# Optimization experiments

Measured on AMD Instinct MI355X. Metric: run time of the kernel, lower is better.

The kernel has to match this reference:

```python
import jax, jax.numpy as jnp
import numpy as np


def setup_inputs() -> dict:
    key = jax.random.key(0)
    ks = jax.random.split(key, 6)
    B, H, N, BS, W, T, D = 1, 32, 256, 32, 128, 4096, 128
    q = jax.random.normal(ks[0], (B, H, N * BS, D), dtype=jnp.float32)
    k_ctx = jax.random.normal(ks[1], (B, H, T, D), dtype=jnp.float32)
    v_ctx = jax.random.normal(ks[2], (B, H, T, D), dtype=jnp.float32)
    k_draft = jax.random.normal(ks[3], (B, H, N * BS, D), dtype=jnp.float32)
    v_draft = jax.random.normal(ks[4], (B, H, N * BS, D), dtype=jnp.float32)
    anchor_positions = jnp.sort(
        jax.random.randint(ks[5], (B, N), 0, T - BS), axis=-1
    )
    block_keep_mask = jnp.ones((B, N), dtype=bool)
    return {
        "q": q, "k_ctx": k_ctx, "v_ctx": v_ctx,
        "k_draft": k_draft, "v_draft": v_draft,
        "anchor_positions": anchor_positions,
        "block_keep_mask": block_keep_mask,
        "context_window": 128,
    }


def reference(q, k_ctx, v_ctx, k_draft, v_draft,
              anchor_positions, block_keep_mask, context_window):
    # FlashMTP block-sparse attention (FlexAttention mask_mod semantics):
    #   query block i attends to context tokens t in [max(0, a_i - W), a_i - 1]
    #   plus its own draft block (bidirectional); invalid blocks see nothing.
    B, H, Q, D = q.shape
    N = anchor_positions.shape[1]
    bs = Q // N
    T = k_ctx.shape[2]
    W = context_window
    scale = 1.0 / np.sqrt(D).astype(np.float32)

    # sliding context window indices per block: (B, N, W)
    idx = anchor_positions[:, :, None] - W + jnp.arange(W)[None, None, :]
    valid_ctx = idx >= 0  # idx < anchor always holds by construction
    idxc = jnp.clip(idx, 0, T - 1)
    gidx = idxc.reshape(B, 1, N * W, 1)
    k_win = jnp.take_along_axis(k_ctx, gidx, axis=2).reshape(B, H, N, W, D)
    v_win = jnp.take_along_axis(v_ctx, gidx, axis=2).reshape(B, H, N, W, D)

    qb = q.reshape(B, H, N, bs, D)
    kb = k_draft.reshape(B, H, N, bs, D)
    vb = v_draft.reshape(B, H, N, bs, D)

    s_ctx = jnp.einsum('bhnqd,bhnwd->bhnqw', qb, k_win) * scale
    s_blk = jnp.einsum('bhnqd,bhnkd->bhnqk', qb, kb) * scale

    keep = block_keep_mask[:, None, :, None, None]           # (B,1,N,1,1)
    m_ctx = valid_ctx[:, None, :, None, :] & keep            # (B,1,N,1,W)
    m_blk = jnp.broadcast_to(keep, (B, 1, N, 1, bs))         # (B,1,N,1,bs)
    mask = jnp.concatenate([m_ctx, m_blk], axis=-1)
    s = jnp.concatenate([s_ctx, s_blk], axis=-1)
    neg = jnp.asarray(-1e30, s.dtype)
    p = jax.nn.softmax(jnp.where(mask, s, neg), axis=-1)

    v_all = jnp.concatenate([v_win, vb], axis=3)             # (B,H,N,W+bs,D)
    out = jnp.einsum('bhnqk,bhnkd->bhnqd', p, v_all)
    out = out * keep.astype(out.dtype)  # invalid blocks -> zero output
    return out.reshape(B, H, Q, D)
```

## Files before the change

kernel.cpp:

```cpp
#include <hip/hip_runtime.h>

constexpr int H_  = 32;
constexpr int N_  = 256;
constexpr int BS_ = 32;
constexpr int W_  = 128;
constexpr int T_  = 4096;
constexpr int D_  = 128;
constexpr int NQ_ = 8192;
constexpr float SCALE_  = 0.08838834764831845f;
constexpr float L2E_    = 1.4426950408889634f;
constexpr float MFLOOR_ = -1.0e28f;
constexpr float DEFER_  = 8.0f;

typedef __attribute__((ext_vector_type(4))) float f4;
typedef __attribute__((ext_vector_type(4))) short s4;
typedef __attribute__((ext_vector_type(8))) short s8;
typedef __attribute__((ext_vector_type(4))) float fx4;

__device__ __forceinline__ short bfrne(float f) {
  unsigned u = __float_as_uint(f);
  u += 0x7fffu + ((u >> 16) & 1u);
  return (short)(u >> 16);
}

__device__ __forceinline__ void lds_barrier() {
  asm volatile("s_waitcnt lgkmcnt(0)" ::: "memory");
  __builtin_amdgcn_s_barrier();
}

__global__ __launch_bounds__(128, 2)
void mtp_attn_kernel(const float* __restrict__ q,
                     const float* __restrict__ k_ctx,
                     const float* __restrict__ v_ctx,
                     const float* __restrict__ k_draft,
                     const float* __restrict__ v_draft,
                     const int* __restrict__ anchor,
                     const int* __restrict__ keepm,
                     float* __restrict__ out)
{
  int u = blockIdx.x;
  u = (u & 7) * 1024 + (u >> 3);
  const int h = u >> 8;
  const int n = u & 255;

  const int tu   = threadIdx.x;
  const int lane = tu & 63;
  const int wu   = tu >> 6;
  const int l15  = lane & 15;
  const int g    = lane >> 4;
  const int rb   = tu >> 5;
  const int c4   = tu & 31;

  const int A  = anchor[n];
  const int kp = keepm[n];
  const int wm = W_ - A;

  __shared__ __align__(16) unsigned char smem_[17664];
  short* kb = (short*)smem_;
  short* vT = (short*)(smem_ + 8448);

  const float* qrow = q + ((size_t)h * NQ_ + (size_t)n * BS_ + wu * 16 + l15) * D_;
  s8 qb[4];
#pragma unroll
  for (int ks = 0; ks < 4; ++ks) {
    f4 f0 = *reinterpret_cast<const f4*>(qrow + ks * 32 + g * 4);
    f4 f1 = *reinterpret_cast<const f4*>(qrow + ks * 32 + 16 + g * 4);
#pragma unroll
    for (int j = 0; j < 4; ++j) { qb[ks][j] = bfrne(f0[j]); qb[ks][j + 4] = bfrne(f1[j]); }
  }

  const float* kcb = k_ctx + (size_t)h * T_ * D_;
  const float* vcb = v_ctx + (size_t)h * T_ * D_;
  const float* kdb = k_draft + ((size_t)h * NQ_ + (size_t)n * BS_) * D_;
  const float* vdb = v_draft + ((size_t)h * NQ_ + (size_t)n * BS_) * D_;

  f4 kr[8], vr[8];

  auto loadK = [&](int c) {
#pragma unroll
    for (int i = 0; i < 8; ++i) {
      int row = i * 4 + rb;
      const float* src;
      if (c < 4) { int idx = A - W_ + c * 32 + row; idx = idx < 0 ? 0 : idx; src = kcb + (size_t)idx * D_; }
      else       { src = kdb + (size_t)row * D_; }
      kr[i] = reinterpret_cast<const f4*>(src)[c4];
    }
  };
  auto loadV = [&](int c) {
#pragma unroll
    for (int p = 0; p < 2; ++p)
#pragma unroll
      for (int i = 0; i < 4; ++i) {
        int row = p * 16 + rb * 4 + i;
        const float* src;
        if (c < 4) { int idx = A - W_ + c * 32 + row; idx = idx < 0 ? 0 : idx; src = vcb + (size_t)idx * D_; }
        else       { src = vdb + (size_t)row * D_; }
        vr[p * 4 + i] = reinterpret_cast<const f4*>(src)[c4];
      }
  };

  loadK(0); loadV(0);

  float m  = -3.0e38f;
  float ls = 0.0f;
  fx4 oacc[8];
#pragma unroll
  for (int t = 0; t < 8; ++t) oacc[t] = {0.f, 0.f, 0.f, 0.f};

#pragma unroll
  for (int c = 0; c < 5; ++c) {
    lds_barrier();
#pragma unroll
    for (int i = 0; i < 8; ++i) {
      s4 w = { bfrne(kr[i][0]), bfrne(kr[i][1]), bfrne(kr[i][2]), bfrne(kr[i][3]) };
      *reinterpret_cast<s4*>(kb + (i * 4 + rb) * 132 + c4 * 4) = w;
    }
#pragma unroll
    for (int p = 0; p < 2; ++p) {
      int keyl = p * 16 + rb * 4;
#pragma unroll
      for (int j = 0; j < 4; ++j) {
        s4 w = { bfrne(vr[p * 4 + 0][j]), bfrne(vr[p * 4 + 1][j]),
                 bfrne(vr[p * 4 + 2][j]), bfrne(vr[p * 4 + 3][j]) };
        *reinterpret_cast<s4*>(vT + (c4 * 4 + j) * 36 + keyl) = w;
      }
    }
    if (c < 4) { loadK(c + 1); loadV(c + 1); }
    lds_barrier();

    fx4 st[2] = { {0.f,0.f,0.f,0.f}, {0.f,0.f,0.f,0.f} };
    __builtin_amdgcn_s_setprio(1);
#pragma unroll
    for (int ks = 0; ks < 4; ++ks) {
#pragma unroll
      for (int t2 = 0; t2 < 2; ++t2) {
        const short* kpr = kb + (t2 * 16 + l15) * 132 + ks * 32 + g * 4;
        s4 b0 = *reinterpret_cast<const s4*>(kpr);
        s4 b1 = *reinterpret_cast<const s4*>(kpr + 16);
        s8 kf = { b0[0], b0[1], b0[2], b0[3], b1[0], b1[1], b1[2], b1[3] };
        st[t2] = __builtin_amdgcn_mfma_f32_16x16x32_bf16(kf, qb[ks], st[t2], 0, 0, 0);
      }
    }
    __builtin_amdgcn_s_setprio(0);

    float sv[2][4];
    float cm = -3.0e38f;
#pragma unroll
    for (int t2 = 0; t2 < 2; ++t2) {
      int kb0 = c * 32 + t2 * 16 + g * 4;
#pragma unroll
      for (int r = 0; r < 4; ++r) {
        float v = st[t2][r] * SCALE_;
        bool valid = (c == 4) || (kb0 + r >= wm);
        v = valid ? v : -1.0e30f;
        sv[t2][r] = v;
        cm = fmaxf(cm, v);
      }
    }
    cm = fmaxf(cm, __shfl_xor(cm, 16));
    cm = fmaxf(cm, __shfl_xor(cm, 32));

    if (c == 0) {
      m = fmaxf(cm, MFLOOR_);
    } else {
      float pm = fmaxf(m, cm);
      if (!__all(pm - m <= DEFER_)) {
        float mn = fmaxf(pm, MFLOOR_);
        float al = exp2f((m - mn) * L2E_);
        ls *= al;
        float alr[4];
#pragma unroll
        for (int r = 0; r < 4; ++r) alr[r] = __shfl(al, g * 4 + r);
#pragma unroll
        for (int nt = 0; nt < 8; ++nt)
#pragma unroll
          for (int r = 0; r < 4; ++r) oacc[nt][r] *= alr[r];
        m = mn;
      }
    }

    s8 pa;
#pragma unroll
    for (int t2 = 0; t2 < 2; ++t2)
#pragma unroll
      for (int r = 0; r < 4; ++r) {
        float p = exp2f((sv[t2][r] - m) * L2E_);
        ls += p;
        pa[t2 * 4 + r] = bfrne(p);
      }

    __builtin_amdgcn_s_setprio(1);
#pragma unroll
    for (int nt = 0; nt < 8; ++nt) {
      const short* vp = vT + (nt * 16 + l15) * 36 + g * 4;
      s4 b0 = *reinterpret_cast<const s4*>(vp);
      s4 b1 = *reinterpret_cast<const s4*>(vp + 16);
      s8 vb2 = { b0[0], b0[1], b0[2], b0[3], b1[0], b1[1], b1[2], b1[3] };
      oacc[nt] = __builtin_amdgcn_mfma_f32_16x16x32_bf16(pa, vb2, oacc[nt], 0, 0, 0);
    }
    __builtin_amdgcn_s_setprio(0);
  }

  ls += __shfl_xor(ls, 16);
  ls += __shfl_xor(ls, 32);
  float linv[4];
#pragma unroll
  for (int r = 0; r < 4; ++r) {
    float lq = __shfl(ls, g * 4 + r);
    linv[r] = kp ? (1.0f / lq) : 0.0f;
  }
  float* ob = out + ((size_t)h * NQ_ + (size_t)n * BS_ + wu * 16 + g * 4) * D_ + l15;
#pragma unroll
  for (int nt = 0; nt < 8; ++nt)
#pragma unroll
    for (int r = 0; r < 4; ++r)
      ob[(size_t)r * D_ + nt * 16] = oacc[nt][r] * linv[r];
}

extern "C" void kernel_launch(void* const* d_in, const int* in_sizes, int n_in,
                              void* d_out, int out_size, void* d_ws, size_t ws_size,
                              hipStream_t stream) {
  (void)in_sizes; (void)n_in; (void)d_ws; (void)ws_size; (void)out_size;
  const float* q       = (const float*)d_in[0];
  const float* k_ctx   = (const float*)d_in[1];
  const float* v_ctx   = (const float*)d_in[2];
  const float* k_draft = (const float*)d_in[3];
  const float* v_draft = (const float*)d_in[4];
  const int*   anchor  = (const int*)d_in[5];
  const int*   keep    = (const int*)d_in[6];
  float*       out     = (float*)d_out;
  mtp_attn_kernel<<<dim3(8192), dim3(128), 0, stream>>>(
      q, k_ctx, v_ctx, k_draft, v_draft, anchor, keep, out);
}
```

Baseline: 159.5 us.

## Double-buffer K/V register prefetch two chunks ahead and use packed bf16 conversion

```diff
diff --git a/kernel.cpp b/kernel.cpp
--- a/kernel.cpp
+++ b/kernel.cpp
@@ -16,12 +16,15 @@
 typedef __attribute__((ext_vector_type(4))) short s4;
 typedef __attribute__((ext_vector_type(8))) short s8;
 typedef __attribute__((ext_vector_type(4))) float fx4;
-
-__device__ __forceinline__ short bfrne(float f) {
-  unsigned u = __float_as_uint(f);
-  u += 0x7fffu + ((u >> 16) & 1u);
-  return (short)(u >> 16);
-}
+typedef __attribute__((ext_vector_type(2))) int i2;
+
+__device__ __forceinline__ int pack2(float a, float b) {
+  int r;
+  asm("v_cvt_pk_bf16_f32 %0, %1, %2" : "=v"(r) : "v"(a), "v"(b));
+  return r;
+}
+
+union frag_u { int w[4]; s8 v; };
 
 __device__ __forceinline__ void lds_barrier() {
   asm volatile("s_waitcnt lgkmcnt(0)" ::: "memory");
@@ -65,8 +68,10 @@
   for (int ks = 0; ks < 4; ++ks) {
     f4 f0 = *reinterpret_cast<const f4*>(qrow + ks * 32 + g * 4);
     f4 f1 = *reinterpret_cast<const f4*>(qrow + ks * 32 + 16 + g * 4);
-#pragma unroll
-    for (int j = 0; j < 4; ++j) { qb[ks][j] = bfrne(f0[j]); qb[ks][j + 4] = bfrne(f1[j]); }
+    frag_u uq;
+    uq.w[0] = pack2(f0[0], f0[1]); uq.w[1] = pack2(f0[2], f0[3]);
+    uq.w[2] = pack2(f1[0], f1[1]); uq.w[3] = pack2(f1[2], f1[3]);
+    qb[ks] = uq.v;
   }
 
   const float* kcb = k_ctx + (size_t)h * T_ * D_;
@@ -74,19 +79,17 @@
   const float* kdb = k_draft + ((size_t)h * NQ_ + (size_t)n * BS_) * D_;
   const float* vdb = v_draft + ((size_t)h * NQ_ + (size_t)n * BS_) * D_;
 
-  f4 kr[8], vr[8];
-
-  auto loadK = [&](int c) {
+  auto loadK = [&](f4 (&dst)[8], int c) {
 #pragma unroll
     for (int i = 0; i < 8; ++i) {
       int row = i * 4 + rb;
       const float* src;
       if (c < 4) { int idx = A - W_ + c * 32 + row; idx = idx < 0 ? 0 : idx; src = kcb + (size_t)idx * D_; }
       else       { src = kdb + (size_t)row * D_; }
-      kr[i] = reinterpret_cast<const f4*>(src)[c4];
+      dst[i] = reinterpret_cast<const f4*>(src)[c4];
     }
   };
-  auto loadV = [&](int c) {
+  auto loadV = [&](f4 (&dst)[8], int c) {
 #pragma unroll
     for (int p = 0; p < 2; ++p)
 #pragma unroll
@@ -95,11 +98,13 @@
         const float* src;
         if (c < 4) { int idx = A - W_ + c * 32 + row; idx = idx < 0 ? 0 : idx; src = vcb + (size_t)idx * D_; }
         else       { src = vdb + (size_t)row * D_; }
-        vr[p * 4 + i] = reinterpret_cast<const f4*>(src)[c4];
+        dst[p * 4 + i] = reinterpret_cast<const f4*>(src)[c4];
       }
   };
 
-  loadK(0); loadV(0);
+  f4 krA[8], vrA[8], krB[8], vrB[8];
+  loadK(krA, 0); loadV(vrA, 0);
+  loadK(krB, 1); loadV(vrB, 1);
 
   float m  = -3.0e38f;
   float ls = 0.0f;
@@ -109,23 +114,26 @@
 
 #pragma unroll
   for (int c = 0; c < 5; ++c) {
+    f4 (&kr)[8] = (c & 1) ? krB : krA;
+    f4 (&vr)[8] = (c & 1) ? vrB : vrA;
+
     lds_barrier();
 #pragma unroll
     for (int i = 0; i < 8; ++i) {
-      s4 w = { bfrne(kr[i][0]), bfrne(kr[i][1]), bfrne(kr[i][2]), bfrne(kr[i][3]) };
-      *reinterpret_cast<s4*>(kb + (i * 4 + rb) * 132 + c4 * 4) = w;
+      i2 w = { pack2(kr[i][0], kr[i][1]), pack2(kr[i][2], kr[i][3]) };
+      *reinterpret_cast<i2*>(kb + (i * 4 + rb) * 132 + c4 * 4) = w;
     }
 #pragma unroll
     for (int p = 0; p < 2; ++p) {
       int keyl = p * 16 + rb * 4;
 #pragma unroll
       for (int j = 0; j < 4; ++j) {
-        s4 w = { bfrne(vr[p * 4 + 0][j]), bfrne(vr[p * 4 + 1][j]),
-                 bfrne(vr[p * 4 + 2][j]), bfrne(vr[p * 4 + 3][j]) };
-        *reinterpret_cast<s4*>(vT + (c4 * 4 + j) * 36 + keyl) = w;
-      }
-    }
-    if (c < 4) { loadK(c + 1); loadV(c + 1); }
+        i2 w = { pack2(vr[p * 4 + 0][j], vr[p * 4 + 1][j]),
+                 pack2(vr[p * 4 + 2][j], vr[p * 4 + 3][j]) };
+        *reinterpret_cast<i2*>(vT + (c4 * 4 + j) * 36 + keyl) = w;
+      }
+    }
+    if (c < 3) { loadK(kr, c + 2); loadV(vr, c + 2); }
     lds_barrier();
 
     fx4 st[2] = { {0.f,0.f,0.f,0.f}, {0.f,0.f,0.f,0.f} };
@@ -179,15 +187,19 @@
       }
     }
 
-    s8 pa;
+    float pv[8];
 #pragma unroll
     for (int t2 = 0; t2 < 2; ++t2)
 #pragma unroll
       for (int r = 0; r < 4; ++r) {
         float p = exp2f((sv[t2][r] - m) * L2E_);
         ls += p;
-        pa[t2 * 4 + r] = bfrne(p);
-      }
+        pv[t2 * 4 + r] = p;
+      }
+    frag_u up;
+    up.w[0] = pack2(pv[0], pv[1]); up.w[1] = pack2(pv[2], pv[3]);
+    up.w[2] = pack2(pv[4], pv[5]); up.w[3] = pack2(pv[6], pv[7]);
+    s8 pa = up.v;
 
     __builtin_amdgcn_s_setprio(1);
 #pragma unroll
```

New measurement: 158.2 us. Within noise of the previous version (-0.8%).
